# Kernel optimization log

Measured on AMD Instinct MI355X. Metric: run time of the kernel, lower is better.

## Reference

```python
import jax, jax.numpy as jnp
import numpy as np
from jax.scipy.linalg import expm

N_QUBITS = 10
DIM = 2 ** N_QUBITS        # 1024, statevector dimension
N_GATES = 24
FEAT_LEN = 1000            # padded with zeros up to DIM (pad_with=0.0)


def setup_inputs() -> dict:
    key = jax.random.key(0)
    kf, kt, kr, ki = jax.random.split(key, 4)
    feature = jax.random.normal(kf, (FEAT_LEN,), dtype=jnp.float32)
    # theta param: (len(gate_indices), 1) as in nn.param('theta', ..., (K, 1))
    theta = jax.random.normal(kt, (N_GATES, 1), dtype=jnp.float32)
    # fixed ansatz generators (Hermitian after symmetrization in reference)
    gens_re = jax.random.normal(kr, (N_GATES, DIM, DIM), dtype=jnp.float32)
    gens_im = jax.random.normal(ki, (N_GATES, DIM, DIM), dtype=jnp.float32)
    return {"feature": feature, "theta": theta, "gens_re": gens_re, "gens_im": gens_im}


def reference(feature, theta, gens_re, gens_im):
    D = gens_re.shape[-1]
    # Hermitian generators G_k = (M + M^H)/2
    M = gens_re.astype(jnp.complex64) + 1j * gens_im.astype(jnp.complex64)
    G = 0.5 * (M + jnp.conj(jnp.swapaxes(M, -1, -2)))  # [K, D, D]

    # AmplitudeEmbedding: pad feature with zeros to D, then L2-normalize
    psi = jnp.zeros((D,), dtype=jnp.complex64)
    psi = psi.at[: feature.shape[0]].set(feature.astype(jnp.complex64))
    psi = psi / jnp.linalg.norm(psi)

    # U_k = expm(-1j * theta_k * G_k), batched over gates
    coeff = (-1j) * theta[:, 0].astype(jnp.complex64)  # [K]
    U = jax.vmap(expm)(coeff[:, None, None] * G)       # [K, D, D]

    # sequential application of gates to the state
    def step(p, Uk):
        return Uk @ p, None

    psi, _ = jax.lax.scan(step, psi, U)

    # qml.probs over all wires
    probs = jnp.abs(psi) ** 2
    return probs
```

## Files before the change

kernel.cpp:

```cpp
#include <hip/hip_runtime.h>
#include <math.h>

#define DIM      1024
#define K_GATES  24
#define NMAX     512
#define QUAD_M   2048
#define BBOUND   66.0f
#define ROWS     16
#define NBLOCKS  64
#define NTHREADS 1024
#define PSLOT    8
#define CANARY   0x7FBADEAD7FBADEADull

union F2U { unsigned long long u; float2 f; };

__device__ __forceinline__ unsigned long long ld64coh(const unsigned long long* p) {
    return __hip_atomic_load(p, __ATOMIC_RELAXED, __HIP_MEMORY_SCOPE_AGENT);
}
__device__ __forceinline__ void st64coh(unsigned long long* p, unsigned long long v) {
    __hip_atomic_store(p, v, __ATOMIC_RELAXED, __HIP_MEMORY_SCOPE_AGENT);
}

__global__ __launch_bounds__(1024) void init_state(const float* __restrict__ f,
                                                   int nfeat,
                                                   unsigned long long* __restrict__ slots) {
    __shared__ float red[16];
    __shared__ float invn_s;
    int t = threadIdx.x;
    float v = (t < nfeat) ? f[t] : 0.f;
    float s = v * v;
    #pragma unroll
    for (int o = 1; o < 64; o <<= 1) s += __shfl_xor(s, o);
    if ((t & 63) == 0) red[t >> 6] = s;
    __syncthreads();
    if (t == 0) {
        float tot = 0.f;
        for (int i = 0; i < 16; i++) tot += red[i];
        invn_s = 1.0f / sqrtf(tot);
    }
    __syncthreads();
    F2U c; c.f = make_float2(v * invn_s, 0.f);
    slots[t] = c.u;
    #pragma unroll
    for (int p = 1; p < PSLOT; p++) slots[(size_t)p * DIM + t] = CANARY;
}

__global__ __launch_bounds__(256) void bessel_coef(const float* __restrict__ theta,
                                                   float2* __restrict__ coefs) {
    int n = blockIdx.x;
    int k = blockIdx.y;
    double tau = (double)theta[k] * (double)BBOUND;
    int t = threadIdx.x;
    double acc = 0.0;
    #pragma unroll
    for (int i = 0; i < QUAD_M / 256; i++) {
        int j = t + 256 * i;
        double phi = (2.0 * M_PI / (double)QUAD_M) * (double)j;
        acc += cos((double)n * phi - tau * sin(phi));
    }
    #pragma unroll
    for (int o = 1; o < 64; o <<= 1) acc += __shfl_xor(acc, o);
    __shared__ double red[4];
    if ((t & 63) == 0) red[t >> 6] = acc;
    __syncthreads();
    if (t == 0) {
        double J = (red[0] + red[1] + red[2] + red[3]) / (double)QUAD_M;
        double f = (n == 0) ? 1.0 : 2.0;
        float cr = 0.f, cim = 0.f;
        switch (n & 3) {
            case 0: cr  =  (float)(f * J); break;
            case 1: cim = -(float)(f * J); break;
            case 2: cr  = -(float)(f * J); break;
            case 3: cim =  (float)(f * J); break;
        }
        coefs[k * NMAX + n] = make_float2(cr, cim);
    }
}

__global__ __launch_bounds__(NMAX) void trunc_len(const float2* __restrict__ coefs,
                                                  int* __restrict__ nterm) {
    int k = blockIdx.x;
    int t = threadIdx.x;
    float2 c = coefs[k * NMAX + t];
    float mag = fabsf(c.x) + fabsf(c.y);
    int myn = (mag > 5e-7f) ? t : 0;
    #pragma unroll
    for (int o = 1; o < 64; o <<= 1) myn = max(myn, __shfl_xor(myn, o));
    __shared__ int red[8];
    if ((t & 63) == 0) red[t >> 6] = myn;
    __syncthreads();
    if (t == 0) {
        int m = 1;
        for (int i = 0; i < 8; i++) m = max(m, red[i]);
        nterm[k] = min(m, NMAX - 1);
    }
}

__global__ __launch_bounds__(NTHREADS) void evolve(
        const float* __restrict__ gre, const float* __restrict__ gim,
        unsigned long long* __restrict__ slots,
        const float2* __restrict__ coefs, const int* __restrict__ nterm,
        float* __restrict__ out) {
    __shared__ float2 Gs[ROWS * DIM];
    __shared__ float2 xs[2 * DIM];
    const int t = threadIdx.x, b = blockIdx.x;
    const int wave = t >> 6, lane = t & 63;
    const int r0 = b * ROWS;
    const int r = r0 + wave;
    const float hB = 0.5f / BBOUND;

    float2 acc = make_float2(0.f, 0.f);
    float2 t_m1 = acc, t_m2 = acc;
    int rho = 1;

    for (int k = 0; k < K_GATES; k++) {
        const float* R = gre + (size_t)k * DIM * DIM;
        const float* I = gim + (size_t)k * DIM * DIM;

        {
            const float4* Rc = (const float4*)(R + (size_t)t * DIM + r0);
            const float4* Ic = (const float4*)(I + (size_t)t * DIM + r0);
            float4 ra0 = Rc[0], ra1 = Rc[1], ra2 = Rc[2], ra3 = Rc[3];
            float4 ia0 = Ic[0], ia1 = Ic[1], ia2 = Ic[2], ia3 = Ic[3];
            Gs[ 0 * DIM + t] = make_float2(hB * ra0.x, -hB * ia0.x);
            Gs[ 1 * DIM + t] = make_float2(hB * ra0.y, -hB * ia0.y);
            Gs[ 2 * DIM + t] = make_float2(hB * ra0.z, -hB * ia0.z);
            Gs[ 3 * DIM + t] = make_float2(hB * ra0.w, -hB * ia0.w);
            Gs[ 4 * DIM + t] = make_float2(hB * ra1.x, -hB * ia1.x);
            Gs[ 5 * DIM + t] = make_float2(hB * ra1.y, -hB * ia1.y);
            Gs[ 6 * DIM + t] = make_float2(hB * ra1.z, -hB * ia1.z);
            Gs[ 7 * DIM + t] = make_float2(hB * ra1.w, -hB * ia1.w);
            Gs[ 8 * DIM + t] = make_float2(hB * ra2.x, -hB * ia2.x);
            Gs[ 9 * DIM + t] = make_float2(hB * ra2.y, -hB * ia2.y);
            Gs[10 * DIM + t] = make_float2(hB * ra2.z, -hB * ia2.z);
            Gs[11 * DIM + t] = make_float2(hB * ra2.w, -hB * ia2.w);
            Gs[12 * DIM + t] = make_float2(hB * ra3.x, -hB * ia3.x);
            Gs[13 * DIM + t] = make_float2(hB * ra3.y, -hB * ia3.y);
            Gs[14 * DIM + t] = make_float2(hB * ra3.z, -hB * ia3.z);
            Gs[15 * DIM + t] = make_float2(hB * ra3.w, -hB * ia3.w);
        }
        __syncthreads();
        {
            const float4* Rr = (const float4*)(R + (size_t)r * DIM);
            const float4* Ir = (const float4*)(I + (size_t)r * DIM);
            float4* G4 = (float4*)(Gs + (size_t)wave * DIM);
            #pragma unroll
            for (int m = 0; m < 4; m++) {
                int i4 = lane + 64 * m;
                float4 rv = Rr[i4], iv = Ir[i4];
                float4 g0 = G4[2 * i4], g1 = G4[2 * i4 + 1];
                g0.x += hB * rv.x; g0.y += hB * iv.x;
                g0.z += hB * rv.y; g0.w += hB * iv.y;
                g1.x += hB * rv.z; g1.y += hB * iv.z;
                g1.z += hB * rv.w; g1.w += hB * iv.w;
                G4[2 * i4] = g0; G4[2 * i4 + 1] = g1;
            }
        }
        __syncthreads();

        const int N = nterm[k];
        const float2* C = coefs + (size_t)k * NMAX;

        for (int n = 1; n <= N + 1; ++n, ++rho) {
            unsigned long long* src = slots + (size_t)((rho - 1) & (PSLOT - 1)) * DIM;
            unsigned long long* dst = slots + (size_t)(rho & (PSLOT - 1)) * DIM;
            unsigned long long* ra  = slots + (size_t)((rho - 2) & (PSLOT - 1)) * DIM;
            float2* xsb = xs + (size_t)(rho & 1) * DIM;

            unsigned long long u = ld64coh(src + t);
            while (u == CANARY) u = ld64coh(src + t);
            { F2U c; c.u = u; xsb[t] = c.f; }
            __syncthreads();

            if (t < ROWS) st64coh(ra + r0 + t, CANARY);

            float2 pub;
            if (n <= N) {
                float sre = 0.f, sim = 0.f;
                const float4* x4 = (const float4*)xsb;
                const float4* g4 = (const float4*)(Gs + (size_t)wave * DIM);
                #pragma unroll
                for (int m = 0; m < 8; m++) {
                    int idx = lane + 64 * m;
                    float4 xv = x4[idx];
                    float4 gv = g4[idx];
                    sre += gv.x * xv.x - gv.y * xv.y + gv.z * xv.z - gv.w * xv.w;
                    sim += gv.x * xv.y + gv.y * xv.x + gv.z * xv.w + gv.w * xv.z;
                }
                #pragma unroll
                for (int o = 1; o < 64; o <<= 1) {
                    sre += __shfl_xor(sre, o);
                    sim += __shfl_xor(sim, o);
                }

                float2 tn;
                if (n == 1) {
                    tn = make_float2(sre, sim);
                    float2 p0 = xsb[r];
                    const float2 c0 = C[0], c1 = C[1];
                    acc.x = c0.x * p0.x - c0.y * p0.y + c1.x * tn.x - c1.y * tn.y;
                    acc.y = c0.x * p0.y + c0.y * p0.x + c1.x * tn.y + c1.y * tn.x;
                    t_m2 = p0;
                } else {
                    tn = make_float2(2.f * sre - t_m2.x, 2.f * sim - t_m2.y);
                    const float2 cn = C[n];
                    acc.x += cn.x * tn.x - cn.y * tn.y;
                    acc.y += cn.x * tn.y + cn.y * tn.x;
                    t_m2 = t_m1;
                }
                t_m1 = tn;
                pub = tn;
            } else {
                pub = acc;
            }

            if (lane == 0) { F2U c; c.f = pub; st64coh(dst + r, c.u); }
        }
    }

    if (lane == 0) out[r] = acc.x * acc.x + acc.y * acc.y;
}

extern "C" void kernel_launch(void* const* d_in, const int* in_sizes, int n_in,
                              void* d_out, int out_size, void* d_ws, size_t ws_size,
                              hipStream_t stream) {
    const float* feat  = (const float*)d_in[0];
    const float* theta = (const float*)d_in[1];
    const float* gre   = (const float*)d_in[2];
    const float* gim   = (const float*)d_in[3];

    char* base = (char*)d_ws;
    unsigned long long* slots = (unsigned long long*)base;
    float2* coefs = (float2*)(base + (size_t)PSLOT * DIM * sizeof(unsigned long long));
    int*    nterm = (int*)(base + (size_t)PSLOT * DIM * sizeof(unsigned long long)
                           + (size_t)K_GATES * NMAX * sizeof(float2));
    float* outp = (float*)d_out;

    init_state<<<1, 1024, 0, stream>>>(feat, in_sizes[0], slots);
    bessel_coef<<<dim3(NMAX, K_GATES), 256, 0, stream>>>(theta, coefs);
    trunc_len<<<K_GATES, NMAX, 0, stream>>>(coefs, nterm);

    void* args[] = {(void*)&gre, (void*)&gim, (void*)&slots,
                    (void*)&coefs, (void*)&nterm, (void*)&outp};
    hipLaunchCooperativeKernel((void*)evolve, dim3(NBLOCKS), dim3(NTHREADS),
                               args, 0, stream);
}
```

Before: 8.074 ms.

## Add hierarchical atomic barrier, cache generator rows in registers, drop extra publish step

Each Chebyshev step now ends with a two-level atomic counter barrier (groups of 8 blocks, then a root counter). Threads keep spinning on canary polling but exit once the barrier releases. The per-gate extra iteration that only republished the accumulator is removed: the last term writes acc directly. The generator row slice is held in registers instead of being reread from LDS each step. The aim is to cut global polling traffic and per-step latency, at the cost of atomic contention and a more delicate slot-recycling protocol.

After: 9.691 ms. 1.2x slower.

```diff
diff --git a/kernel.cpp b/kernel.cpp
--- a/kernel.cpp
+++ b/kernel.cpp
@@ -23,7 +23,8 @@
 
 __global__ __launch_bounds__(1024) void init_state(const float* __restrict__ f,
                                                    int nfeat,
-                                                   unsigned long long* __restrict__ slots) {
+                                                   unsigned long long* __restrict__ slots,
+                                                   unsigned int* __restrict__ bars) {
     __shared__ float red[16];
     __shared__ float invn_s;
     int t = threadIdx.x;
@@ -43,6 +44,7 @@
     slots[t] = c.u;
     #pragma unroll
     for (int p = 1; p < PSLOT; p++) slots[(size_t)p * DIM + t] = CANARY;
+    if (t < 160) bars[t] = 0u;
 }
 
 __global__ __launch_bounds__(256) void bessel_coef(const float* __restrict__ theta,
@@ -100,23 +102,30 @@
         const float* __restrict__ gre, const float* __restrict__ gim,
         unsigned long long* __restrict__ slots,
         const float2* __restrict__ coefs, const int* __restrict__ nterm,
-        float* __restrict__ out) {
+        unsigned int* __restrict__ bars, float* __restrict__ out) {
     __shared__ float2 Gs[ROWS * DIM];
-    __shared__ float2 xs[2 * DIM];
+    __shared__ float2 xs[2][DIM];
+    __shared__ int go_tag;
     const int t = threadIdx.x, b = blockIdx.x;
     const int wave = t >> 6, lane = t & 63;
     const int r0 = b * ROWS;
     const int r = r0 + wave;
     const float hB = 0.5f / BBOUND;
-
+    unsigned int* grp  = bars + (b >> 3) * 16;
+    unsigned int* root = bars + 8 * 16;
+
+    { F2U c; c.u = ld64coh(slots + t); xs[0][t] = c.f; }
+    if (t == 0) go_tag = 0;
     float2 acc = make_float2(0.f, 0.f);
-    float2 t_m1 = acc, t_m2 = acc;
+    float2 t1 = acc, t2 = acc;
     int rho = 1;
-
-    for (int k = 0; k < K_GATES; k++) {
+    __syncthreads();
+
+    for (int k = 0; k < K_GATES; ++k) {
         const float* R = gre + (size_t)k * DIM * DIM;
         const float* I = gim + (size_t)k * DIM * DIM;
 
+        __syncthreads();
         {
             const float4* Rc = (const float4*)(R + (size_t)t * DIM + r0);
             const float4* Ic = (const float4*)(I + (size_t)t * DIM + r0);
@@ -157,64 +166,77 @@
             }
         }
         __syncthreads();
+        float4 gq[8];
+        #pragma unroll
+        for (int m = 0; m < 8; ++m)
+            gq[m] = *(const float4*)(Gs + (size_t)wave * DIM + 2 * (lane + 64 * m));
 
         const int N = nterm[k];
         const float2* C = coefs + (size_t)k * NMAX;
 
-        for (int n = 1; n <= N + 1; ++n, ++rho) {
-            unsigned long long* src = slots + (size_t)((rho - 1) & (PSLOT - 1)) * DIM;
+        for (int n = 1; n <= N; ++n, ++rho) {
             unsigned long long* dst = slots + (size_t)(rho & (PSLOT - 1)) * DIM;
-            unsigned long long* ra  = slots + (size_t)((rho - 2) & (PSLOT - 1)) * DIM;
-            float2* xsb = xs + (size_t)(rho & 1) * DIM;
-
-            unsigned long long u = ld64coh(src + t);
-            while (u == CANARY) u = ld64coh(src + t);
-            { F2U c; c.u = u; xsb[t] = c.f; }
+            const float2* xsrc = xs[(rho - 1) & 1];
+
+            float sre = 0.f, sim = 0.f;
+            const float4* x4 = (const float4*)xsrc;
+            #pragma unroll
+            for (int m = 0; m < 8; ++m) {
+                float4 xv = x4[lane + 64 * m];
+                float4 gv = gq[m];
+                sre += gv.x * xv.x - gv.y * xv.y + gv.z * xv.z - gv.w * xv.w;
+                sim += gv.x * xv.y + gv.y * xv.x + gv.z * xv.w + gv.w * xv.z;
+            }
+            #pragma unroll
+            for (int o = 1; o < 64; o <<= 1) {
+                sre += __shfl_xor(sre, o);
+                sim += __shfl_xor(sim, o);
+            }
+
+            float2 tn;
+            if (n == 1) {
+                tn = make_float2(sre, sim);
+                const float2 p0 = xsrc[r];
+                const float2 c0 = C[0], c1 = C[1];
+                acc.x = c0.x * p0.x - c0.y * p0.y + c1.x * tn.x - c1.y * tn.y;
+                acc.y = c0.x * p0.y + c0.y * p0.x + c1.x * tn.y + c1.y * tn.x;
+                t2 = p0;
+            } else {
+                tn = make_float2(2.f * sre - t2.x, 2.f * sim - t2.y);
+                const float2 cn = C[n];
+                acc.x += cn.x * tn.x - cn.y * tn.y;
+                acc.y += cn.x * tn.y + cn.y * tn.x;
+                t2 = t1;
+            }
+            t1 = tn;
+            const float2 res = (n == N) ? acc : tn;
+
+            if (lane == 0) { F2U c; c.f = res; st64coh(dst + r, c.u); }
             __syncthreads();
 
-            if (t < ROWS) st64coh(ra + r0 + t, CANARY);
-
-            float2 pub;
-            if (n <= N) {
-                float sre = 0.f, sim = 0.f;
-                const float4* x4 = (const float4*)xsb;
-                const float4* g4 = (const float4*)(Gs + (size_t)wave * DIM);
-                #pragma unroll
-                for (int m = 0; m < 8; m++) {
-                    int idx = lane + 64 * m;
-                    float4 xv = x4[idx];
-                    float4 gv = g4[idx];
-                    sre += gv.x * xv.x - gv.y * xv.y + gv.z * xv.z - gv.w * xv.w;
-                    sim += gv.x * xv.y + gv.y * xv.x + gv.z * xv.w + gv.w * xv.z;
-                }
-                #pragma unroll
-                for (int o = 1; o < 64; o <<= 1) {
-                    sre += __shfl_xor(sre, o);
-                    sim += __shfl_xor(sim, o);
-                }
-
-                float2 tn;
-                if (n == 1) {
-                    tn = make_float2(sre, sim);
-                    float2 p0 = xsb[r];
-                    const float2 c0 = C[0], c1 = C[1];
-                    acc.x = c0.x * p0.x - c0.y * p0.y + c1.x * tn.x - c1.y * tn.y;
-                    acc.y = c0.x * p0.y + c0.y * p0.x + c1.x * tn.y + c1.y * tn.x;
-                    t_m2 = p0;
-                } else {
-                    tn = make_float2(2.f * sre - t_m2.x, 2.f * sim - t_m2.y);
-                    const float2 cn = C[n];
-                    acc.x += cn.x * tn.x - cn.y * tn.y;
-                    acc.y += cn.x * tn.y + cn.y * tn.x;
-                    t_m2 = t_m1;
-                }
-                t_m1 = tn;
-                pub = tn;
-            } else {
-                pub = acc;
-            }
-
-            if (lane == 0) { F2U c; c.f = pub; st64coh(dst + r, c.u); }
+            unsigned long long u = ld64coh(dst + t);
+
+            if (t == 0) {
+                unsigned old = __hip_atomic_fetch_add(grp, 1u, __ATOMIC_RELAXED,
+                                                      __HIP_MEMORY_SCOPE_AGENT);
+                if ((old & 7u) == 7u)
+                    __hip_atomic_fetch_add(root, 1u, __ATOMIC_RELAXED,
+                                           __HIP_MEMORY_SCOPE_AGENT);
+                while (__hip_atomic_load(root, __ATOMIC_RELAXED,
+                                         __HIP_MEMORY_SCOPE_AGENT) < 8u * (unsigned)rho)
+                    __builtin_amdgcn_s_sleep(1);
+                *(volatile int*)&go_tag = rho;
+            }
+            while (u == CANARY && *(volatile int*)&go_tag != rho)
+                u = ld64coh(dst + t);
+            while (u == CANARY) u = ld64coh(dst + t);
+
+            { F2U c; c.u = u; xs[rho & 1][t] = c.f; }
+            __syncthreads();
+
+            if (t < ROWS)
+                st64coh(slots + (size_t)((rho - 1) & (PSLOT - 1)) * DIM + r0 + t,
+                        CANARY);
         }
     }
 
@@ -231,17 +253,21 @@
 
     char* base = (char*)d_ws;
     unsigned long long* slots = (unsigned long long*)base;
-    float2* coefs = (float2*)(base + (size_t)PSLOT * DIM * sizeof(unsigned long long));
-    int*    nterm = (int*)(base + (size_t)PSLOT * DIM * sizeof(unsigned long long)
-                           + (size_t)K_GATES * NMAX * sizeof(float2));
+    size_t off = (size_t)PSLOT * DIM * sizeof(unsigned long long);
+    float2* coefs = (float2*)(base + off);
+    off += (size_t)K_GATES * NMAX * sizeof(float2);
+    int* nterm = (int*)(base + off);
+    off += (size_t)K_GATES * sizeof(int);
+    off = (off + 255) & ~(size_t)255;
+    unsigned int* bars = (unsigned int*)(base + off);
     float* outp = (float*)d_out;
 
-    init_state<<<1, 1024, 0, stream>>>(feat, in_sizes[0], slots);
+    init_state<<<1, 1024, 0, stream>>>(feat, in_sizes[0], slots, bars);
     bessel_coef<<<dim3(NMAX, K_GATES), 256, 0, stream>>>(theta, coefs);
     trunc_len<<<K_GATES, NMAX, 0, stream>>>(coefs, nterm);
 
     void* args[] = {(void*)&gre, (void*)&gim, (void*)&slots,
-                    (void*)&coefs, (void*)&nterm, (void*)&outp};
+                    (void*)&coefs, (void*)&nterm, (void*)&bars, (void*)&outp};
     hipLaunchCooperativeKernel((void*)evolve, dim3(NBLOCKS), dim3(NTHREADS),
                                args, 0, stream);
 }
```
